# Kernel optimization log

Measured on AMD Instinct MI355X. Metric: run time of the kernel, lower is better.

The kernel has to match this reference:

```python
import jax, jax.numpy as jnp
import numpy as np

WS = (8, 8)  # window_size
NUM_HEADS = 6


def _relative_position_index(ws):
    ch, cw = np.arange(ws[0]), np.arange(ws[1])
    coords = np.stack(np.meshgrid(ch, cw, indexing='ij'))  # [2, Wh, Ww]
    cf = coords.reshape(2, -1)  # [2, N]
    rel = cf[:, :, None] - cf[:, None, :]  # [2, N, N]
    rel = rel.transpose(1, 2, 0).astype(np.int64)
    rel[:, :, 0] += ws[0] - 1
    rel[:, :, 1] += ws[1] - 1
    rel[:, :, 0] *= 2 * ws[1] - 1
    return rel.sum(-1)  # [N, N]

_RPI = jnp.asarray(_relative_position_index(WS))  # [64, 64] int


def setup_inputs() -> dict:
    key = jax.random.key(0)
    ks = jax.random.split(key, 6)
    B_, N, C = 4096, WS[0] * WS[1], 192
    return {
        'x': jax.random.normal(ks[0], (B_, N, C), jnp.float32),
        'qkv_w': jax.random.normal(ks[1], (3 * C, C), jnp.float32) * 0.02,
        'qkv_b': jax.random.normal(ks[2], (3 * C,), jnp.float32) * 0.02,
        'proj_w': jax.random.normal(ks[3], (C, C), jnp.float32) * 0.02,
        'proj_b': jax.random.normal(ks[4], (C,), jnp.float32) * 0.02,
        'rpb_table': jax.random.normal(ks[5], ((2 * WS[0] - 1) * (2 * WS[1] - 1), NUM_HEADS), jnp.float32) * 0.02,
    }


def reference(x, qkv_w, qkv_b, proj_w, proj_b, rpb_table):
    B_, N, C = x.shape
    H = NUM_HEADS
    D = C // H
    scale = D ** (-0.5)
    # qkv: torch Linear -> x @ W^T + b
    qkv = (x @ qkv_w.T + qkv_b).reshape(B_, N, 3, H, D)
    qkv = jnp.transpose(qkv, (2, 0, 3, 1, 4))  # [3, B_, H, N, D]
    q, k, v = qkv[0] * scale, qkv[1], qkv[2]
    attn = jnp.einsum('bhnd,bhmd->bhnm', q, k)  # [B_, H, N, N]
    bias = rpb_table[_RPI]  # [N, N, H]
    attn = attn + jnp.transpose(bias, (2, 0, 1))[None]  # broadcast over B_
    attn = jax.nn.softmax(attn, axis=-1)
    out = jnp.einsum('bhnm,bhmd->bnhd', attn, v).reshape(B_, N, C)
    return out @ proj_w.T + proj_b
```

## Files before the change

kernel.cpp:

```cpp
#include <hip/hip_runtime.h>

typedef short bf16x8 __attribute__((ext_vector_type(8)));
typedef float f32x4 __attribute__((ext_vector_type(4)));
typedef unsigned int u32;

#define MFMA16 __builtin_amdgcn_mfma_f32_16x16x32_bf16

#define SCALE 0.17677669529663687f


__device__ __forceinline__ unsigned short f2b(float x) {
  u32 u = __float_as_uint(x);
  u = (u + 0x7FFFu + ((u >> 16) & 1u)) >> 16;
  return (unsigned short)u;
}
__device__ __forceinline__ u32 pk2(float a, float b) {
  u32 ua = __float_as_uint(a), ub = __float_as_uint(b);
  ua = (ua + 0x7FFFu + ((ua >> 16) & 1u)) >> 16;
  ub = (ub + 0x7FFFu + ((ub >> 16) & 1u)) >> 16;
  return (ua & 0xFFFFu) | (ub << 16);
}

__global__ void prep_kernel(const float* __restrict__ qkv_w, const float* __restrict__ qkv_b,
                            const float* __restrict__ proj_w, const float* __restrict__ rpb,
                            unsigned short* __restrict__ wqkv, unsigned short* __restrict__ wproj,
                            float* __restrict__ biasar, float* __restrict__ bq) {
  int i0 = blockIdx.x * blockDim.x + threadIdx.x;
  int stride = gridDim.x * blockDim.x;
  for (int i = i0; i < 576 * 192; i += stride) {
    float v = qkv_w[i];
    if (i < 192 * 192) v *= SCALE;
    wqkv[i] = f2b(v);
  }
  for (int i = i0; i < 192 * 192; i += stride) wproj[i] = f2b(proj_w[i]);
  for (int i = i0; i < 576; i += stride) {
    float v = qkv_b[i];
    if (i < 192) v *= SCALE;
    bq[i] = v;
  }
  for (int i = i0; i < 6 * 16 * 64 * 4; i += stride) {
    int r = i & 3;
    int lane = (i >> 2) & 63;
    int fid = (i >> 8) & 15;
    int h = i >> 12;
    int mt = fid >> 2, nt = fid & 3;
    int m = mt * 16 + (lane >> 4) * 4 + r;
    int n = nt * 16 + (lane & 15);
    int idx = ((n >> 3) - (m >> 3) + 7) * 15 + ((n & 7) - (m & 7) + 7);
    biasar[i] = rpb[idx * 6 + h];
  }
}

__global__ void __launch_bounds__(384) win_attn(
    const float* __restrict__ x, const unsigned short* __restrict__ wqkv,
    const unsigned short* __restrict__ wproj, const float* __restrict__ biasar,
    const float* __restrict__ bq, const float* __restrict__ proj_b, float* __restrict__ out) {
  __shared__ __align__(16) char smem[44032];
  const int b = blockIdx.x;
  const int tid = threadIdx.x;
  const int w = tid >> 6;
  const int lane = tid & 63;
  const int g = lane >> 4;
  const int c = lane & 15;
  char* scr = smem + 13312 + w * 5120;

  f32x4 accQ[2][4], accK[2][4], accV[4][2];
#pragma unroll
  for (int a = 0; a < 2; ++a)
#pragma unroll
    for (int t = 0; t < 4; ++t) {
      accQ[a][t] = (f32x4)0.0f;
      accK[a][t] = (f32x4)0.0f;
      accV[t][a] = (f32x4)0.0f;
    }

  for (int ck = 0; ck < 2; ++ck) {
    {
      const float* xb = x + (size_t)b * 12288 + ck * 96;
#pragma unroll
      for (int it = 0; it < 4; ++it) {
        int idx = tid + it * 384;
        int tok = idx / 24, c4 = idx % 24;
        float4 v = *(const float4*)(xb + tok * 192 + c4 * 4);
        *(uint2*)(smem + tok * 208 + c4 * 8) = make_uint2(pk2(v.x, v.y), pk2(v.z, v.w));
      }
    }
    __syncthreads();
#pragma unroll
    for (int kt = 0; kt < 3; ++kt) {
      int cb = ck * 96 + kt * 32 + 8 * g;
      bf16x8 wqf[2], wkf[2], wvf[2];
#pragma unroll
      for (int dt = 0; dt < 2; ++dt) {
        int fr = w * 32 + dt * 16 + c;
        wqf[dt] = *(const bf16x8*)(wqkv + (size_t)fr * 192 + cb);
        wkf[dt] = *(const bf16x8*)(wqkv + (size_t)(192 + fr) * 192 + cb);
        wvf[dt] = *(const bf16x8*)(wqkv + (size_t)(384 + fr) * 192 + cb);
      }
#pragma unroll
      for (int tt = 0; tt < 4; ++tt) {
        bf16x8 xf = *(const bf16x8*)(smem + (tt * 16 + c) * 208 + (kt * 32 + 8 * g) * 2);
#pragma unroll
        for (int dt = 0; dt < 2; ++dt) {
          accQ[dt][tt] = MFMA16(wqf[dt], xf, accQ[dt][tt], 0, 0, 0);
          accK[dt][tt] = MFMA16(wkf[dt], xf, accK[dt][tt], 0, 0, 0);
          accV[tt][dt] = MFMA16(xf, wvf[dt], accV[tt][dt], 0, 0, 0);
        }
      }
    }
    __syncthreads();
  }

#pragma unroll
  for (int dt = 0; dt < 2; ++dt)
#pragma unroll
    for (int r = 0; r < 4; ++r) {
      float bqv = bq[w * 32 + dt * 16 + 4 * g + r];
      float bkv = bq[192 + w * 32 + dt * 16 + 4 * g + r];
#pragma unroll
      for (int tt = 0; tt < 4; ++tt) {
        accQ[dt][tt][r] += bqv;
        accK[dt][tt][r] += bkv;
      }
    }
#pragma unroll
  for (int dt = 0; dt < 2; ++dt) {
    float bvv = bq[384 + w * 32 + dt * 16 + c];
#pragma unroll
    for (int mt = 0; mt < 4; ++mt)
#pragma unroll
      for (int r = 0; r < 4; ++r) accV[mt][dt][r] += bvv;
  }

  bf16x8 qb[4], ka[4], va[2][2];
#pragma unroll
  for (int dt = 0; dt < 2; ++dt)
#pragma unroll
    for (int nt = 0; nt < 4; ++nt)
      *(uint2*)(scr + (nt * 16 + c) * 80 + (dt * 16 + 4 * g) * 2) =
          make_uint2(pk2(accQ[dt][nt][0], accQ[dt][nt][1]), pk2(accQ[dt][nt][2], accQ[dt][nt][3]));
#pragma unroll
  for (int nt = 0; nt < 4; ++nt) qb[nt] = *(const bf16x8*)(scr + (nt * 16 + c) * 80 + 16 * g);
#pragma unroll
  for (int dt = 0; dt < 2; ++dt)
#pragma unroll
    for (int mt = 0; mt < 4; ++mt)
      *(uint2*)(scr + (mt * 16 + c) * 80 + (dt * 16 + 4 * g) * 2) =
          make_uint2(pk2(accK[dt][mt][0], accK[dt][mt][1]), pk2(accK[dt][mt][2], accK[dt][mt][3]));
#pragma unroll
  for (int mt = 0; mt < 4; ++mt) ka[mt] = *(const bf16x8*)(scr + (mt * 16 + c) * 80 + 16 * g);
#pragma unroll
  for (int mt = 0; mt < 4; ++mt)
#pragma unroll
    for (int dt = 0; dt < 2; ++dt)
      *(uint2*)(scr + (dt * 16 + c) * 144 + (mt * 16 + 4 * g) * 2) =
          make_uint2(pk2(accV[mt][dt][0], accV[mt][dt][1]), pk2(accV[mt][dt][2], accV[mt][dt][3]));
#pragma unroll
  for (int dt = 0; dt < 2; ++dt)
#pragma unroll
    for (int kt = 0; kt < 2; ++kt)
      va[dt][kt] = *(const bf16x8*)(scr + (dt * 16 + c) * 144 + (kt * 32 + 8 * g) * 2);

  f32x4 s[4][4];
#pragma unroll
  for (int mt = 0; mt < 4; ++mt)
#pragma unroll
    for (int nt = 0; nt < 4; ++nt) s[mt][nt] = (f32x4)0.0f;
#pragma unroll
  for (int mt = 0; mt < 4; ++mt)
#pragma unroll
    for (int nt = 0; nt < 4; ++nt) s[mt][nt] = MFMA16(ka[mt], qb[nt], s[mt][nt], 0, 0, 0);
  const f32x4* bias4 = (const f32x4*)biasar;
#pragma unroll
  for (int mt = 0; mt < 4; ++mt)
#pragma unroll
    for (int nt = 0; nt < 4; ++nt) s[mt][nt] += bias4[(w * 16 + mt * 4 + nt) * 64 + lane];

  float linv[4];
#pragma unroll
  for (int nt = 0; nt < 4; ++nt) {
    float mx = -1e30f;
#pragma unroll
    for (int mt = 0; mt < 4; ++mt)
#pragma unroll
      for (int r = 0; r < 4; ++r) mx = fmaxf(mx, s[mt][nt][r]);
    mx = fmaxf(mx, __shfl_xor(mx, 16));
    mx = fmaxf(mx, __shfl_xor(mx, 32));
    float sum = 0.0f;
#pragma unroll
    for (int mt = 0; mt < 4; ++mt)
#pragma unroll
      for (int r = 0; r < 4; ++r) {
        float e = __expf(s[mt][nt][r] - mx);
        s[mt][nt][r] = e;
        sum += e;
      }
    sum += __shfl_xor(sum, 16);
    sum += __shfl_xor(sum, 32);
    linv[nt] = 1.0f / sum;
  }

  f32x4 o[2][4];
#pragma unroll
  for (int dt = 0; dt < 2; ++dt)
#pragma unroll
    for (int nt = 0; nt < 4; ++nt) o[dt][nt] = (f32x4)0.0f;
#pragma unroll
  for (int half = 0; half < 2; ++half) {
#pragma unroll
    for (int mt2 = 0; mt2 < 2; ++mt2) {
      int mt = half * 2 + mt2;
#pragma unroll
      for (int nt = 0; nt < 4; ++nt)
        *(uint2*)(scr + (nt * 16 + c) * 80 + (mt2 * 16 + 4 * g) * 2) =
            make_uint2(pk2(s[mt][nt][0], s[mt][nt][1]), pk2(s[mt][nt][2], s[mt][nt][3]));
    }
#pragma unroll
    for (int nt = 0; nt < 4; ++nt) {
      bf16x8 pb = *(const bf16x8*)(scr + (nt * 16 + c) * 80 + 16 * g);
#pragma unroll
      for (int dt = 0; dt < 2; ++dt) o[dt][nt] = MFMA16(va[dt][half], pb, o[dt][nt], 0, 0, 0);
    }
  }
#pragma unroll
  for (int dt = 0; dt < 2; ++dt)
#pragma unroll
    for (int nt = 0; nt < 4; ++nt)
#pragma unroll
      for (int r = 0; r < 4; ++r) o[dt][nt][r] *= linv[nt];

  __syncthreads();
#pragma unroll
  for (int dt = 0; dt < 2; ++dt)
#pragma unroll
    for (int nt = 0; nt < 4; ++nt)
      *(uint2*)(smem + (nt * 16 + c) * 400 + (w * 32 + dt * 16 + 4 * g) * 2) =
          make_uint2(pk2(o[dt][nt][0], o[dt][nt][1]), pk2(o[dt][nt][2], o[dt][nt][3]));
  __syncthreads();

  f32x4 accP[4][2];
#pragma unroll
  for (int mt = 0; mt < 4; ++mt)
#pragma unroll
    for (int ft = 0; ft < 2; ++ft) accP[mt][ft] = (f32x4)0.0f;
#pragma unroll
  for (int kt = 0; kt < 6; ++kt) {
    bf16x8 wp[2];
#pragma unroll
    for (int ft = 0; ft < 2; ++ft)
      wp[ft] = *(const bf16x8*)(wproj + (size_t)(w * 32 + ft * 16 + c) * 192 + kt * 32 + 8 * g);
#pragma unroll
    for (int mt = 0; mt < 4; ++mt) {
      bf16x8 of = *(const bf16x8*)(smem + (mt * 16 + c) * 400 + (kt * 32 + 8 * g) * 2);
#pragma unroll
      for (int ft = 0; ft < 2; ++ft) accP[mt][ft] = MFMA16(of, wp[ft], accP[mt][ft], 0, 0, 0);
    }
  }
  float pb0 = proj_b[w * 32 + c];
  float pb1 = proj_b[w * 32 + 16 + c];
  float* outb = out + (size_t)b * 12288;
#pragma unroll
  for (int mt = 0; mt < 4; ++mt)
#pragma unroll
    for (int ft = 0; ft < 2; ++ft) {
      float pbv = ft ? pb1 : pb0;
#pragma unroll
      for (int r = 0; r < 4; ++r)
        outb[(mt * 16 + 4 * g + r) * 192 + w * 32 + ft * 16 + c] = accP[mt][ft][r] + pbv;
    }
}

extern "C" void kernel_launch(void* const* d_in, const int* in_sizes, int n_in,
                              void* d_out, int out_size, void* d_ws, size_t ws_size,
                              hipStream_t stream) {
  const float* x = (const float*)d_in[0];
  const float* qkv_w = (const float*)d_in[1];
  const float* qkv_b = (const float*)d_in[2];
  const float* proj_w = (const float*)d_in[3];
  const float* proj_b = (const float*)d_in[4];
  const float* rpb = (const float*)d_in[5];
  char* ws = (char*)d_ws;
  unsigned short* wqkv = (unsigned short*)ws;
  unsigned short* wproj = (unsigned short*)(ws + 221184);
  float* biasar = (float*)(ws + 294912);
  float* bqv = (float*)(ws + 393216);

  prep_kernel<<<432, 256, 0, stream>>>(qkv_w, qkv_b, proj_w, rpb, wqkv, wproj, biasar, bqv);
  win_attn<<<4096, 384, 0, stream>>>(x, wqkv, wproj, biasar, bqv, proj_b, (float*)d_out);
}
```

Measured before the change: 305.7 us.

## Stage full x tile with XOR swizzle, split QKV GEMMs to cut register pressure

Loads the whole 64x192 input tile into shared memory once, using an XOR-swizzled layout in place of padded rows, which removes the two-chunk loop and its barriers. Q, K and V projections are now computed in sequence, and softmax runs on half-tiles, so far fewer accumulators are live at once. Launch bounds ask for 5 blocks per SM. Packing now uses the HIP bf16 intrinsic. Shared memory grows to 48KB, which may cap occupancy, and the weights are reloaded across three separate passes.

```diff
diff --git a/kernel.cpp b/kernel.cpp
--- a/kernel.cpp
+++ b/kernel.cpp
@@ -1,11 +1,11 @@
 #include <hip/hip_runtime.h>
+#include <hip/hip_bf16.h>
 
 typedef short bf16x8 __attribute__((ext_vector_type(8)));
 typedef float f32x4 __attribute__((ext_vector_type(4)));
 typedef unsigned int u32;
 
 #define MFMA16 __builtin_amdgcn_mfma_f32_16x16x32_bf16
-
 #define SCALE 0.17677669529663687f
 
 
@@ -15,10 +15,11 @@
   return (unsigned short)u;
 }
 __device__ __forceinline__ u32 pk2(float a, float b) {
-  u32 ua = __float_as_uint(a), ub = __float_as_uint(b);
-  ua = (ua + 0x7FFFu + ((ua >> 16) & 1u)) >> 16;
-  ub = (ub + 0x7FFFu + ((ub >> 16) & 1u)) >> 16;
-  return (ua & 0xFFFFu) | (ub << 16);
+  __hip_bfloat162 h = __float22bfloat162_rn(float2{a, b});
+  return *(u32*)&h;
+}
+__device__ __forceinline__ uint2 pk4(f32x4 v) {
+  return make_uint2(pk2(v[0], v[1]), pk2(v[2], v[3]));
 }
 
 __global__ void prep_kernel(const float* __restrict__ qkv_w, const float* __restrict__ qkv_b,
@@ -51,191 +52,234 @@
   }
 }
 
-__global__ void __launch_bounds__(384) win_attn(
+__global__ void __launch_bounds__(384, 5) win_attn(
     const float* __restrict__ x, const unsigned short* __restrict__ wqkv,
     const unsigned short* __restrict__ wproj, const float* __restrict__ biasar,
     const float* __restrict__ bq, const float* __restrict__ proj_b, float* __restrict__ out) {
-  __shared__ __align__(16) char smem[44032];
+  __shared__ __align__(16) char smem[49152];
   const int b = blockIdx.x;
   const int tid = threadIdx.x;
   const int w = tid >> 6;
   const int lane = tid & 63;
   const int g = lane >> 4;
   const int c = lane & 15;
-  char* scr = smem + 13312 + w * 5120;
-
-  f32x4 accQ[2][4], accK[2][4], accV[4][2];
-#pragma unroll
-  for (int a = 0; a < 2; ++a)
-#pragma unroll
-    for (int t = 0; t < 4; ++t) {
-      accQ[a][t] = (f32x4)0.0f;
-      accK[a][t] = (f32x4)0.0f;
-      accV[t][a] = (f32x4)0.0f;
-    }
-
-  for (int ck = 0; ck < 2; ++ck) {
-    {
-      const float* xb = x + (size_t)b * 12288 + ck * 96;
-#pragma unroll
-      for (int it = 0; it < 4; ++it) {
-        int idx = tid + it * 384;
-        int tok = idx / 24, c4 = idx % 24;
-        float4 v = *(const float4*)(xb + tok * 192 + c4 * 4);
-        *(uint2*)(smem + tok * 208 + c4 * 8) = make_uint2(pk2(v.x, v.y), pk2(v.z, v.w));
-      }
-    }
-    __syncthreads();
-#pragma unroll
-    for (int kt = 0; kt < 3; ++kt) {
-      int cb = ck * 96 + kt * 32 + 8 * g;
-      bf16x8 wqf[2], wkf[2], wvf[2];
-#pragma unroll
-      for (int dt = 0; dt < 2; ++dt) {
-        int fr = w * 32 + dt * 16 + c;
-        wqf[dt] = *(const bf16x8*)(wqkv + (size_t)fr * 192 + cb);
-        wkf[dt] = *(const bf16x8*)(wqkv + (size_t)(192 + fr) * 192 + cb);
-        wvf[dt] = *(const bf16x8*)(wqkv + (size_t)(384 + fr) * 192 + cb);
-      }
+  char* xs = smem;
+  char* scr = smem + 24576 + w * 4096;
+
+  {
+    const float* xb = x + (size_t)b * 12288;
+#pragma unroll
+    for (int it = 0; it < 8; ++it) {
+      int idx = tid + it * 384;
+      int tok = idx / 48, c4 = idx % 48;
+      float4 v = *(const float4*)(xb + tok * 192 + c4 * 4);
+      *(uint2*)(xs + tok * 384 + (((c4 >> 1) ^ (tok & 7)) << 4) + (c4 & 1) * 8) =
+          make_uint2(pk2(v.x, v.y), pk2(v.z, v.w));
+    }
+  }
+  __syncthreads();
+
+#define XFRAG(tt, kt) \
+  (*(const bf16x8*)(xs + ((tt) * 16 + c) * 384 + ((((kt) * 4 + g) ^ (c & 7)) << 4)))
+
+  bf16x8 qb[4];
+  {
+    f32x4 acc[2][4];
+#pragma unroll
+    for (int dt = 0; dt < 2; ++dt)
+#pragma unroll
+      for (int tt = 0; tt < 4; ++tt) acc[dt][tt] = (f32x4)0.0f;
+#pragma unroll
+    for (int kt = 0; kt < 6; ++kt) {
+      bf16x8 wf[2];
+#pragma unroll
+      for (int dt = 0; dt < 2; ++dt)
+        wf[dt] = *(const bf16x8*)(wqkv + (size_t)(w * 32 + dt * 16 + c) * 192 + kt * 32 + 8 * g);
 #pragma unroll
       for (int tt = 0; tt < 4; ++tt) {
-        bf16x8 xf = *(const bf16x8*)(smem + (tt * 16 + c) * 208 + (kt * 32 + 8 * g) * 2);
-#pragma unroll
-        for (int dt = 0; dt < 2; ++dt) {
-          accQ[dt][tt] = MFMA16(wqf[dt], xf, accQ[dt][tt], 0, 0, 0);
-          accK[dt][tt] = MFMA16(wkf[dt], xf, accK[dt][tt], 0, 0, 0);
-          accV[tt][dt] = MFMA16(xf, wvf[dt], accV[tt][dt], 0, 0, 0);
+        bf16x8 xf = XFRAG(tt, kt);
+#pragma unroll
+        for (int dt = 0; dt < 2; ++dt) acc[dt][tt] = MFMA16(wf[dt], xf, acc[dt][tt], 0, 0, 0);
+      }
+    }
+#pragma unroll
+    for (int dt = 0; dt < 2; ++dt)
+#pragma unroll
+      for (int r = 0; r < 4; ++r) {
+        float bv = bq[w * 32 + dt * 16 + 4 * g + r];
+#pragma unroll
+        for (int tt = 0; tt < 4; ++tt) acc[dt][tt][r] += bv;
+      }
+#pragma unroll
+    for (int dt = 0; dt < 2; ++dt)
+#pragma unroll
+      for (int nt = 0; nt < 4; ++nt)
+        *(uint2*)(scr + (nt * 16 + c) * 64 + (((dt * 2 + (g >> 1)) ^ (c & 3)) << 4) + (g & 1) * 8) =
+            pk4(acc[dt][nt]);
+#pragma unroll
+    for (int nt = 0; nt < 4; ++nt)
+      qb[nt] = *(const bf16x8*)(scr + (nt * 16 + c) * 64 + ((g ^ (c & 3)) << 4));
+  }
+
+  bf16x8 ka[4];
+  {
+    f32x4 acc[2][4];
+#pragma unroll
+    for (int dt = 0; dt < 2; ++dt)
+#pragma unroll
+      for (int tt = 0; tt < 4; ++tt) acc[dt][tt] = (f32x4)0.0f;
+#pragma unroll
+    for (int kt = 0; kt < 6; ++kt) {
+      bf16x8 wf[2];
+#pragma unroll
+      for (int dt = 0; dt < 2; ++dt)
+        wf[dt] = *(const bf16x8*)(wqkv + (size_t)(192 + w * 32 + dt * 16 + c) * 192 + kt * 32 + 8 * g);
+#pragma unroll
+      for (int tt = 0; tt < 4; ++tt) {
+        bf16x8 xf = XFRAG(tt, kt);
+#pragma unroll
+        for (int dt = 0; dt < 2; ++dt) acc[dt][tt] = MFMA16(wf[dt], xf, acc[dt][tt], 0, 0, 0);
+      }
+    }
+#pragma unroll
+    for (int dt = 0; dt < 2; ++dt)
+#pragma unroll
+      for (int r = 0; r < 4; ++r) {
+        float bv = bq[192 + w * 32 + dt * 16 + 4 * g + r];
+#pragma unroll
+        for (int tt = 0; tt < 4; ++tt) acc[dt][tt][r] += bv;
+      }
+#pragma unroll
+    for (int dt = 0; dt < 2; ++dt)
+#pragma unroll
+      for (int mt = 0; mt < 4; ++mt)
+        *(uint2*)(scr + (mt * 16 + c) * 64 + (((dt * 2 + (g >> 1)) ^ (c & 3)) << 4) + (g & 1) * 8) =
+            pk4(acc[dt][mt]);
+#pragma unroll
+    for (int mt = 0; mt < 4; ++mt)
+      ka[mt] = *(const bf16x8*)(scr + (mt * 16 + c) * 64 + ((g ^ (c & 3)) << 4));
+  }
+
+  bf16x8 pbf[2][4];
+  float linv[4];
+  const f32x4* bias4 = (const f32x4*)biasar;
+#pragma unroll
+  for (int h = 0; h < 2; ++h) {
+    f32x4 s[4][2];
+#pragma unroll
+    for (int mt = 0; mt < 4; ++mt)
+#pragma unroll
+      for (int n2 = 0; n2 < 2; ++n2) {
+        int nt = h * 2 + n2;
+        f32x4 t = MFMA16(ka[mt], qb[nt], (f32x4)0.0f, 0, 0, 0);
+        s[mt][n2] = t + bias4[(w * 16 + mt * 4 + nt) * 64 + lane];
+      }
+#pragma unroll
+    for (int n2 = 0; n2 < 2; ++n2) {
+      int nt = h * 2 + n2;
+      float mx = -1e30f;
+#pragma unroll
+      for (int mt = 0; mt < 4; ++mt)
+#pragma unroll
+        for (int r = 0; r < 4; ++r) mx = fmaxf(mx, s[mt][n2][r]);
+      mx = fmaxf(mx, __shfl_xor(mx, 16));
+      mx = fmaxf(mx, __shfl_xor(mx, 32));
+      float sum = 0.0f;
+#pragma unroll
+      for (int mt = 0; mt < 4; ++mt)
+#pragma unroll
+        for (int r = 0; r < 4; ++r) {
+          float e = __expf(s[mt][n2][r] - mx);
+          s[mt][n2][r] = e;
+          sum += e;
         }
-      }
-    }
-    __syncthreads();
-  }
-
+      sum += __shfl_xor(sum, 16);
+      sum += __shfl_xor(sum, 32);
+      linv[nt] = 1.0f / sum;
+    }
+#pragma unroll
+    for (int mh = 0; mh < 2; ++mh)
+#pragma unroll
+      for (int mt2 = 0; mt2 < 2; ++mt2)
+#pragma unroll
+        for (int n2 = 0; n2 < 2; ++n2)
+          *(uint2*)(scr + (mh * 32 + n2 * 16 + c) * 64 +
+                    (((mt2 * 2 + (g >> 1)) ^ (c & 3)) << 4) + (g & 1) * 8) =
+              pk4(s[mh * 2 + mt2][n2]);
+#pragma unroll
+    for (int mh = 0; mh < 2; ++mh)
+#pragma unroll
+      for (int n2 = 0; n2 < 2; ++n2)
+        pbf[mh][h * 2 + n2] =
+            *(const bf16x8*)(scr + (mh * 32 + n2 * 16 + c) * 64 + ((g ^ (c & 3)) << 4));
+  }
+
+  bf16x8 va[2][2];
+  {
+    f32x4 acc[4][2];
+#pragma unroll
+    for (int mt = 0; mt < 4; ++mt)
+#pragma unroll
+      for (int dt = 0; dt < 2; ++dt) acc[mt][dt] = (f32x4)0.0f;
+#pragma unroll
+    for (int kt = 0; kt < 6; ++kt) {
+      bf16x8 wf[2];
+#pragma unroll
+      for (int dt = 0; dt < 2; ++dt)
+        wf[dt] = *(const bf16x8*)(wqkv + (size_t)(384 + w * 32 + dt * 16 + c) * 192 + kt * 32 + 8 * g);
+#pragma unroll
+      for (int tt = 0; tt < 4; ++tt) {
+        bf16x8 xf = XFRAG(tt, kt);
+#pragma unroll
+        for (int dt = 0; dt < 2; ++dt) acc[tt][dt] = MFMA16(xf, wf[dt], acc[tt][dt], 0, 0, 0);
+      }
+    }
+#pragma unroll
+    for (int dt = 0; dt < 2; ++dt) {
+      float bv = bq[384 + w * 32 + dt * 16 + c];
+#pragma unroll
+      for (int mt = 0; mt < 4; ++mt)
+#pragma unroll
+        for (int r = 0; r < 4; ++r) acc[mt][dt][r] += bv;
+    }
+#pragma unroll
+    for (int mt = 0; mt < 4; ++mt)
+#pragma unroll
+      for (int dt = 0; dt < 2; ++dt)
+        *(uint2*)(scr + (dt * 16 + c) * 128 + (((mt * 2 + (g >> 1)) ^ (c & 7)) << 4) + (g & 1) * 8) =
+            pk4(acc[mt][dt]);
+#pragma unroll
+    for (int dt = 0; dt < 2; ++dt)
+#pragma unroll
+      for (int kh = 0; kh < 2; ++kh)
+        va[dt][kh] = *(const bf16x8*)(scr + (dt * 16 + c) * 128 + (((kh * 4 + g) ^ (c & 7)) << 4));
+  }
+
+  f32x4 o[2][4];
 #pragma unroll
   for (int dt = 0; dt < 2; ++dt)
 #pragma unroll
-    for (int r = 0; r < 4; ++r) {
-      float bqv = bq[w * 32 + dt * 16 + 4 * g + r];
-      float bkv = bq[192 + w * 32 + dt * 16 + 4 * g + r];
-#pragma unroll
-      for (int tt = 0; tt < 4; ++tt) {
-        accQ[dt][tt][r] += bqv;
-        accK[dt][tt][r] += bkv;
-      }
-    }
-#pragma unroll
-  for (int dt = 0; dt < 2; ++dt) {
-    float bvv = bq[384 + w * 32 + dt * 16 + c];
-#pragma unroll
-    for (int mt = 0; mt < 4; ++mt)
-#pragma unroll
-      for (int r = 0; r < 4; ++r) accV[mt][dt][r] += bvv;
-  }
-
-  bf16x8 qb[4], ka[4], va[2][2];
+    for (int nt = 0; nt < 4; ++nt) o[dt][nt] = (f32x4)0.0f;
+#pragma unroll
+  for (int mh = 0; mh < 2; ++mh)
+#pragma unroll
+    for (int nt = 0; nt < 4; ++nt)
+#pragma unroll
+      for (int dt = 0; dt < 2; ++dt) o[dt][nt] = MFMA16(va[dt][mh], pbf[mh][nt], o[dt][nt], 0, 0, 0);
 #pragma unroll
   for (int dt = 0; dt < 2; ++dt)
 #pragma unroll
     for (int nt = 0; nt < 4; ++nt)
-      *(uint2*)(scr + (nt * 16 + c) * 80 + (dt * 16 + 4 * g) * 2) =
-          make_uint2(pk2(accQ[dt][nt][0], accQ[dt][nt][1]), pk2(accQ[dt][nt][2], accQ[dt][nt][3]));
-#pragma unroll
-  for (int nt = 0; nt < 4; ++nt) qb[nt] = *(const bf16x8*)(scr + (nt * 16 + c) * 80 + 16 * g);
+#pragma unroll
+      for (int r = 0; r < 4; ++r) o[dt][nt][r] *= linv[nt];
+
+  __syncthreads();
 #pragma unroll
   for (int dt = 0; dt < 2; ++dt)
 #pragma unroll
-    for (int mt = 0; mt < 4; ++mt)
-      *(uint2*)(scr + (mt * 16 + c) * 80 + (dt * 16 + 4 * g) * 2) =
-          make_uint2(pk2(accK[dt][mt][0], accK[dt][mt][1]), pk2(accK[dt][mt][2], accK[dt][mt][3]));
-#pragma unroll
-  for (int mt = 0; mt < 4; ++mt) ka[mt] = *(const bf16x8*)(scr + (mt * 16 + c) * 80 + 16 * g);
-#pragma unroll
-  for (int mt = 0; mt < 4; ++mt)
-#pragma unroll
-    for (int dt = 0; dt < 2; ++dt)
-      *(uint2*)(scr + (dt * 16 + c) * 144 + (mt * 16 + 4 * g) * 2) =
-          make_uint2(pk2(accV[mt][dt][0], accV[mt][dt][1]), pk2(accV[mt][dt][2], accV[mt][dt][3]));
-#pragma unroll
-  for (int dt = 0; dt < 2; ++dt)
-#pragma unroll
-    for (int kt = 0; kt < 2; ++kt)
-      va[dt][kt] = *(const bf16x8*)(scr + (dt * 16 + c) * 144 + (kt * 32 + 8 * g) * 2);
-
-  f32x4 s[4][4];
-#pragma unroll
-  for (int mt = 0; mt < 4; ++mt)
-#pragma unroll
-    for (int nt = 0; nt < 4; ++nt) s[mt][nt] = (f32x4)0.0f;
-#pragma unroll
-  for (int mt = 0; mt < 4; ++mt)
-#pragma unroll
-    for (int nt = 0; nt < 4; ++nt) s[mt][nt] = MFMA16(ka[mt], qb[nt], s[mt][nt], 0, 0, 0);
-  const f32x4* bias4 = (const f32x4*)biasar;
-#pragma unroll
-  for (int mt = 0; mt < 4; ++mt)
-#pragma unroll
-    for (int nt = 0; nt < 4; ++nt) s[mt][nt] += bias4[(w * 16 + mt * 4 + nt) * 64 + lane];
-
-  float linv[4];
-#pragma unroll
-  for (int nt = 0; nt < 4; ++nt) {
-    float mx = -1e30f;
-#pragma unroll
-    for (int mt = 0; mt < 4; ++mt)
-#pragma unroll
-      for (int r = 0; r < 4; ++r) mx = fmaxf(mx, s[mt][nt][r]);
-    mx = fmaxf(mx, __shfl_xor(mx, 16));
-    mx = fmaxf(mx, __shfl_xor(mx, 32));
-    float sum = 0.0f;
-#pragma unroll
-    for (int mt = 0; mt < 4; ++mt)
-#pragma unroll
-      for (int r = 0; r < 4; ++r) {
-        float e = __expf(s[mt][nt][r] - mx);
-        s[mt][nt][r] = e;
-        sum += e;
-      }
-    sum += __shfl_xor(sum, 16);
-    sum += __shfl_xor(sum, 32);
-    linv[nt] = 1.0f / sum;
-  }
-
-  f32x4 o[2][4];
-#pragma unroll
-  for (int dt = 0; dt < 2; ++dt)
-#pragma unroll
-    for (int nt = 0; nt < 4; ++nt) o[dt][nt] = (f32x4)0.0f;
-#pragma unroll
-  for (int half = 0; half < 2; ++half) {
-#pragma unroll
-    for (int mt2 = 0; mt2 < 2; ++mt2) {
-      int mt = half * 2 + mt2;
-#pragma unroll
-      for (int nt = 0; nt < 4; ++nt)
-        *(uint2*)(scr + (nt * 16 + c) * 80 + (mt2 * 16 + 4 * g) * 2) =
-            make_uint2(pk2(s[mt][nt][0], s[mt][nt][1]), pk2(s[mt][nt][2], s[mt][nt][3]));
-    }
-#pragma unroll
-    for (int nt = 0; nt < 4; ++nt) {
-      bf16x8 pb = *(const bf16x8*)(scr + (nt * 16 + c) * 80 + 16 * g);
-#pragma unroll
-      for (int dt = 0; dt < 2; ++dt) o[dt][nt] = MFMA16(va[dt][half], pb, o[dt][nt], 0, 0, 0);
-    }
-  }
-#pragma unroll
-  for (int dt = 0; dt < 2; ++dt)
-#pragma unroll
     for (int nt = 0; nt < 4; ++nt)
-#pragma unroll
-      for (int r = 0; r < 4; ++r) o[dt][nt][r] *= linv[nt];
-
-  __syncthreads();
-#pragma unroll
-  for (int dt = 0; dt < 2; ++dt)
-#pragma unroll
-    for (int nt = 0; nt < 4; ++nt)
-      *(uint2*)(smem + (nt * 16 + c) * 400 + (w * 32 + dt * 16 + 4 * g) * 2) =
-          make_uint2(pk2(o[dt][nt][0], o[dt][nt][1]), pk2(o[dt][nt][2], o[dt][nt][3]));
+      *(uint2*)(xs + (nt * 16 + c) * 384 + (((w * 4 + dt * 2 + (g >> 1)) ^ (c & 7)) << 4) +
+                (g & 1) * 8) = pk4(o[dt][nt]);
   __syncthreads();
 
   f32x4 accP[4][2];
@@ -251,7 +295,7 @@
       wp[ft] = *(const bf16x8*)(wproj + (size_t)(w * 32 + ft * 16 + c) * 192 + kt * 32 + 8 * g);
 #pragma unroll
     for (int mt = 0; mt < 4; ++mt) {
-      bf16x8 of = *(const bf16x8*)(smem + (mt * 16 + c) * 400 + (kt * 32 + 8 * g) * 2);
+      bf16x8 of = *(const bf16x8*)(xs + (mt * 16 + c) * 384 + (((kt * 4 + g) ^ (c & 7)) << 4));
 #pragma unroll
       for (int ft = 0; ft < 2; ++ft) accP[mt][ft] = MFMA16(of, wp[ft], accP[mt][ft], 0, 0, 0);
     }
```

Result: faster. 291.5 us (-4.7%).
